# Optimization experiments

Hardware: AMD Instinct MI355X
Metric: run time of the kernel (lower is better)

Reference implementation:

```python
import jax, jax.numpy as jnp
import numpy as np

DIM = 384
RED = 16
PAIR = 128
EPS = 1e-5


def setup_inputs() -> dict:
    key = jax.random.key(0)
    ks = jax.random.split(key, 6)
    b, m = 2, 512
    x = jax.random.normal(ks[0], (b, m, DIM), dtype=jnp.float32)
    ln_gamma = jnp.ones((DIM,), dtype=jnp.float32)
    ln_beta = jnp.zeros((DIM,), dtype=jnp.float32)
    w_red = jax.random.normal(ks[1], (DIM, RED), dtype=jnp.float32) / np.sqrt(DIM)
    b_red = jax.random.normal(ks[2], (RED,), dtype=jnp.float32) * 0.02
    w_out = jax.random.normal(ks[3], (RED * RED, PAIR), dtype=jnp.float32) / np.sqrt(RED * RED)
    b_out = jax.random.normal(ks[4], (PAIR,), dtype=jnp.float32) * 0.02
    return {"x": x, "ln_gamma": ln_gamma, "ln_beta": ln_beta,
            "w_red": w_red, "b_red": b_red, "w_out": w_out, "b_out": b_out}


def reference(x, ln_gamma, ln_beta, w_red, b_red, w_out, b_out):
    # LayerNorm over last dim (eps=1e-5, torch default)
    mu = jnp.mean(x, axis=-1, keepdims=True)
    var = jnp.mean(jnp.square(x - mu), axis=-1, keepdims=True)
    xn = (x - mu) * jax.lax.rsqrt(var + EPS) * ln_gamma + ln_beta
    # Linear dim -> 16
    xr = jnp.einsum('bmd,dr->bmr', xn, w_red) + b_red  # (b, m, 16)
    # Full pairwise outer product + projection: same math as
    # einsum('bmi,bnj->bmnij') -> reshape (i j) -> Linear(256, pair_dim),
    # fused so the (i,j) axes contract directly with w_out reshaped to (16,16,pair).
    wr = w_out.reshape(RED, RED, PAIR)
    out = jnp.einsum('bmi,bnj,ijp->bmnp', xr, xr, wr) + b_out  # (b, m, m, pair)
    return out
```

## Files before the change

### kernel.cpp

```cpp
#include <hip/hip_runtime.h>
#include <hip/hip_bf16.h>

#define DIM 384
#define RED 16
#define PAIR 128
#define B 2
#define M 512
#define EPSV 1e-5f

typedef float f32x4 __attribute__((ext_vector_type(4)));
typedef short bf16x8 __attribute__((ext_vector_type(8)));

__device__ __forceinline__ unsigned short f2bf(float f) {
  union { float f; unsigned u; } v; v.f = f;
  unsigned r = v.u + 0x7fffu + ((v.u >> 16) & 1u);
  return (unsigned short)(r >> 16);
}

__global__ __launch_bounds__(128) void opm_k1(
    const float* __restrict__ x, const float* __restrict__ g,
    const float* __restrict__ be, const float* __restrict__ w_red,
    const float* __restrict__ b_red, const float* __restrict__ w_out,
    unsigned short* __restrict__ xr_bf, unsigned short* __restrict__ T_bf) {
  const int row = blockIdx.x;
  const int tid = threadIdx.x;
  const float* xrow = x + (size_t)row * DIM;

  __shared__ float xn[DIM];
  __shared__ float xr_s[RED];
  __shared__ float rs[2][2];
  __shared__ float psum[8][RED];

  float v0 = xrow[tid];
  float v1 = xrow[tid + 128];
  float v2 = xrow[tid + 256];
  float s  = v0 + v1 + v2;
  float sq = v0 * v0 + v1 * v1 + v2 * v2;
  #pragma unroll
  for (int off = 32; off > 0; off >>= 1) {
    s  += __shfl_down(s, off);
    sq += __shfl_down(sq, off);
  }
  if ((tid & 63) == 0) { rs[0][tid >> 6] = s; rs[1][tid >> 6] = sq; }
  __syncthreads();
  const float mean = (rs[0][0] + rs[0][1]) * (1.0f / DIM);
  const float var  = (rs[1][0] + rs[1][1]) * (1.0f / DIM) - mean * mean;
  const float rstd = rsqrtf(var + EPSV);

  xn[tid]       = (v0 - mean) * rstd * g[tid]       + be[tid];
  xn[tid + 128] = (v1 - mean) * rstd * g[tid + 128] + be[tid + 128];
  xn[tid + 256] = (v2 - mean) * rstd * g[tid + 256] + be[tid + 256];
  __syncthreads();

  {
    const int r = tid & 15;
    const int part = tid >> 4;
    float ps = 0.0f;
    const int d0 = part * 48;
    #pragma unroll 8
    for (int d = d0; d < d0 + 48; ++d) ps += xn[d] * w_red[d * RED + r];
    psum[part][r] = ps;
  }
  __syncthreads();
  if (tid < RED) {
    float v = b_red[tid];
    #pragma unroll
    for (int q = 0; q < 8; ++q) v += psum[q][tid];
    xr_s[tid] = v;
    xr_bf[(size_t)row * RED + tid] = f2bf(v);
  }
  __syncthreads();

  {
    const int p = tid;
    const float* W = w_out + p;
    float acc[RED];
    #pragma unroll
    for (int i = 0; i < RED; ++i) {
      float a = 0.0f;
      #pragma unroll
      for (int j = 0; j < RED; ++j) a += xr_s[j] * W[(i * RED + j) * PAIR];
      acc[i] = a;
    }
    unsigned int w0[4], w1[4];
    #pragma unroll
    for (int k = 0; k < 4; ++k) {
      w0[k] = (unsigned)f2bf(acc[2*k])     | ((unsigned)f2bf(acc[2*k+1]) << 16);
      w1[k] = (unsigned)f2bf(acc[8+2*k])   | ((unsigned)f2bf(acc[8+2*k+1]) << 16);
    }
    unsigned int* dst = (unsigned int*)(T_bf + ((size_t)row * PAIR + p) * RED);
    #pragma unroll
    for (int k = 0; k < 4; ++k) { dst[k] = w0[k]; dst[4+k] = w1[k]; }
  }
}

__global__ __launch_bounds__(256) void opm_k2(
    const unsigned short* __restrict__ xr_bf, const unsigned short* __restrict__ T_bf,
    const float* __restrict__ b_out, float* __restrict__ out) {
  const int nb = blockIdx.x & 127;
  const int mh = (blockIdx.x >> 7) & 1;
  const int b  = blockIdx.x >> 8;
  const int wave = threadIdx.x >> 6;
  const int lane = threadIdx.x & 63;
  const int q = lane >> 4;
  const int r = lane & 15;
  const int n = nb * 4 + wave;

  bf16x8 tv[8];
  const unsigned short* Tb = T_bf + ((size_t)(b * M + n) * PAIR) * RED;
  #pragma unroll
  for (int pb = 0; pb < 8; ++pb) {
    bf16x8 v = {0, 0, 0, 0, 0, 0, 0, 0};
    if (q < 2) v = *(const bf16x8*)(Tb + (pb * 16 + r) * RED + q * 8);
    tv[pb] = v;
  }
  f32x4 biasv[8];
  #pragma unroll
  for (int pb = 0; pb < 8; ++pb)
    biasv[pb] = *(const f32x4*)(b_out + pb * 16 + q * 4);

  const unsigned short* xr_base = xr_bf + (size_t)(b * M) * RED;
  float* out_base = out + ((size_t)(b * M) * M + n) * PAIR + q * 4;

  #pragma unroll
  for (int mt4 = 0; mt4 < 4; ++mt4) {
    const int mt = mh * 4 + mt4;
    #pragma unroll
    for (int ms = 0; ms < 4; ++ms) {
      const int m0 = mt * 64 + ms * 16;
      bf16x8 xv = {0, 0, 0, 0, 0, 0, 0, 0};
      if (q < 2) xv = *(const bf16x8*)(xr_base + (size_t)(m0 + r) * RED + q * 8);

      float* ob = out_base + (size_t)(m0 + r) * M * PAIR;
      #pragma unroll
      for (int pb = 0; pb < 8; ++pb) {
        f32x4 acc = biasv[pb];
        acc = __builtin_amdgcn_mfma_f32_16x16x32_bf16(tv[pb], xv, acc, 0, 0, 0);
        *(f32x4*)(ob + pb * 16) = acc;
      }
    }
  }
}

extern "C" void kernel_launch(void* const* d_in, const int* in_sizes, int n_in,
                              void* d_out, int out_size, void* d_ws, size_t ws_size,
                              hipStream_t stream) {
  const float* x       = (const float*)d_in[0];
  const float* ln_g    = (const float*)d_in[1];
  const float* ln_b    = (const float*)d_in[2];
  const float* w_red   = (const float*)d_in[3];
  const float* b_red   = (const float*)d_in[4];
  const float* w_out   = (const float*)d_in[5];
  const float* b_out   = (const float*)d_in[6];
  float* out = (float*)d_out;

  unsigned short* xr_bf = (unsigned short*)d_ws;
  unsigned short* T_bf  = xr_bf + (size_t)B * M * RED;

  opm_k1<<<B * M, 128, 0, stream>>>(x, ln_g, ln_b, w_red, b_red, w_out, xr_bf, T_bf);
  opm_k2<<<B * (M / 4) * 2, 256, 0, stream>>>(xr_bf, T_bf, b_out, out);
}
```

Measured before the change: 57.45 us.

## Fuse T projection into output kernel via LDS and use wave-per-row LayerNorm

The per-row T = xr·W_out projection moves from the first kernel into the second, where each block builds T for its four n rows in LDS instead of writing it to and reading it back from global workspace. Each T is now computed twice, once per m-half block, in exchange for dropping the T global round trip. The first kernel now handles one row per wave with shuffle-only reductions and no block barriers, and it also writes an fp32 copy of xr for the second kernel.

```diff
diff --git a/kernel.cpp b/kernel.cpp
--- a/kernel.cpp
+++ b/kernel.cpp
@@ -17,101 +17,104 @@
   return (unsigned short)(r >> 16);
 }
 
-__global__ __launch_bounds__(128) void opm_k1(
+__global__ __launch_bounds__(256) void opm_k1(
     const float* __restrict__ x, const float* __restrict__ g,
     const float* __restrict__ be, const float* __restrict__ w_red,
-    const float* __restrict__ b_red, const float* __restrict__ w_out,
-    unsigned short* __restrict__ xr_bf, unsigned short* __restrict__ T_bf) {
-  const int row = blockIdx.x;
-  const int tid = threadIdx.x;
+    const float* __restrict__ b_red,
+    unsigned short* __restrict__ xr_bf, float* __restrict__ xr_f32) {
+  const int wave = threadIdx.x >> 6;
+  const int lane = threadIdx.x & 63;
+  const int row  = blockIdx.x * 4 + wave;
+
+  __shared__ float xn_s[4][DIM];
+
   const float* xrow = x + (size_t)row * DIM;
-
-  __shared__ float xn[DIM];
-  __shared__ float xr_s[RED];
-  __shared__ float rs[2][2];
-  __shared__ float psum[8][RED];
-
-  float v0 = xrow[tid];
-  float v1 = xrow[tid + 128];
-  float v2 = xrow[tid + 256];
-  float s  = v0 + v1 + v2;
-  float sq = v0 * v0 + v1 * v1 + v2 * v2;
+  float v[6];
+  #pragma unroll
+  for (int k = 0; k < 6; ++k) v[k] = xrow[lane + 64 * k];
+  float s = 0.f, sq = 0.f;
+  #pragma unroll
+  for (int k = 0; k < 6; ++k) { s += v[k]; sq += v[k] * v[k]; }
   #pragma unroll
   for (int off = 32; off > 0; off >>= 1) {
-    s  += __shfl_down(s, off);
-    sq += __shfl_down(sq, off);
+    s  += __shfl_xor(s, off);
+    sq += __shfl_xor(sq, off);
   }
-  if ((tid & 63) == 0) { rs[0][tid >> 6] = s; rs[1][tid >> 6] = sq; }
-  __syncthreads();
-  const float mean = (rs[0][0] + rs[0][1]) * (1.0f / DIM);
-  const float var  = (rs[1][0] + rs[1][1]) * (1.0f / DIM) - mean * mean;
+  const float mean = s * (1.0f / DIM);
+  const float var  = sq * (1.0f / DIM) - mean * mean;
   const float rstd = rsqrtf(var + EPSV);
+  #pragma unroll
+  for (int k = 0; k < 6; ++k) {
+    const int d = lane + 64 * k;
+    xn_s[wave][d] = (v[k] - mean) * rstd * g[d] + be[d];
+  }
 
-  xn[tid]       = (v0 - mean) * rstd * g[tid]       + be[tid];
-  xn[tid + 128] = (v1 - mean) * rstd * g[tid + 128] + be[tid + 128];
-  xn[tid + 256] = (v2 - mean) * rstd * g[tid + 256] + be[tid + 256];
-  __syncthreads();
+  const int r = lane & 15, part = lane >> 4;
+  const int d0 = part * 96;
+  float ps = 0.f;
+  #pragma unroll 4
+  for (int d = d0; d < d0 + 96; ++d) ps += xn_s[wave][d] * w_red[d * RED + r];
+  ps += __shfl_xor(ps, 16);
+  ps += __shfl_xor(ps, 32);
+  if (lane < 16) {
+    const float val = ps + b_red[lane];
+    xr_f32[(size_t)row * RED + lane] = val;
+    xr_bf [(size_t)row * RED + lane] = f2bf(val);
+  }
+}
 
-  {
-    const int r = tid & 15;
-    const int part = tid >> 4;
-    float ps = 0.0f;
-    const int d0 = part * 48;
-    #pragma unroll 8
-    for (int d = d0; d < d0 + 48; ++d) ps += xn[d] * w_red[d * RED + r];
-    psum[part][r] = ps;
-  }
-  __syncthreads();
-  if (tid < RED) {
-    float v = b_red[tid];
-    #pragma unroll
-    for (int q = 0; q < 8; ++q) v += psum[q][tid];
-    xr_s[tid] = v;
-    xr_bf[(size_t)row * RED + tid] = f2bf(v);
+__global__ __launch_bounds__(256) void opm_k2(
+    const unsigned short* __restrict__ xr_bf, const float* __restrict__ xr_f32,
+    const float* __restrict__ w_out, const float* __restrict__ b_out,
+    float* __restrict__ out) {
+  const int nb = blockIdx.x & 127;
+  const int mh = (blockIdx.x >> 7) & 1;
+  const int b  = blockIdx.x >> 8;
+  const int tid  = threadIdx.x;
+  const int wave = tid >> 6;
+  const int lane = tid & 63;
+  const int q = lane >> 4;
+  const int r = lane & 15;
+  const int n = nb * 4 + wave;
+
+  __shared__ float xr_lds[4][RED];
+  __shared__ unsigned short T_lds[4][PAIR][RED];
+
+  if (tid < 64) {
+    const int nl = tid >> 4, j = tid & 15;
+    xr_lds[nl][j] = xr_f32[(size_t)(b * M + nb * 4 + nl) * RED + j];
   }
   __syncthreads();
 
   {
-    const int p = tid;
+    const int h2 = tid >> 7;
+    const int p  = tid & 127;
     const float* W = w_out + p;
-    float acc[RED];
+    const float* x0 = xr_lds[2 * h2];
+    const float* x1 = xr_lds[2 * h2 + 1];
+    unsigned int* dst0 = (unsigned int*)&T_lds[2 * h2][p][0];
+    unsigned int* dst1 = (unsigned int*)&T_lds[2 * h2 + 1][p][0];
     #pragma unroll
-    for (int i = 0; i < RED; ++i) {
-      float a = 0.0f;
+    for (int i = 0; i < RED; i += 2) {
+      float a00 = 0.f, a01 = 0.f, a10 = 0.f, a11 = 0.f;
       #pragma unroll
-      for (int j = 0; j < RED; ++j) a += xr_s[j] * W[(i * RED + j) * PAIR];
-      acc[i] = a;
+      for (int j = 0; j < RED; ++j) {
+        const float w0 = W[(i * RED + j) * PAIR];
+        const float w1 = W[((i + 1) * RED + j) * PAIR];
+        a00 += x0[j] * w0;  a01 += x0[j] * w1;
+        a10 += x1[j] * w0;  a11 += x1[j] * w1;
+      }
+      dst0[i >> 1] = (unsigned)f2bf(a00) | ((unsigned)f2bf(a01) << 16);
+      dst1[i >> 1] = (unsigned)f2bf(a10) | ((unsigned)f2bf(a11) << 16);
     }
-    unsigned int w0[4], w1[4];
-    #pragma unroll
-    for (int k = 0; k < 4; ++k) {
-      w0[k] = (unsigned)f2bf(acc[2*k])     | ((unsigned)f2bf(acc[2*k+1]) << 16);
-      w1[k] = (unsigned)f2bf(acc[8+2*k])   | ((unsigned)f2bf(acc[8+2*k+1]) << 16);
-    }
-    unsigned int* dst = (unsigned int*)(T_bf + ((size_t)row * PAIR + p) * RED);
-    #pragma unroll
-    for (int k = 0; k < 4; ++k) { dst[k] = w0[k]; dst[4+k] = w1[k]; }
   }
-}
-
-__global__ __launch_bounds__(256) void opm_k2(
-    const unsigned short* __restrict__ xr_bf, const unsigned short* __restrict__ T_bf,
-    const float* __restrict__ b_out, float* __restrict__ out) {
-  const int nb = blockIdx.x & 127;
-  const int mh = (blockIdx.x >> 7) & 1;
-  const int b  = blockIdx.x >> 8;
-  const int wave = threadIdx.x >> 6;
-  const int lane = threadIdx.x & 63;
-  const int q = lane >> 4;
-  const int r = lane & 15;
-  const int n = nb * 4 + wave;
+  __syncthreads();
 
   bf16x8 tv[8];
-  const unsigned short* Tb = T_bf + ((size_t)(b * M + n) * PAIR) * RED;
   #pragma unroll
   for (int pb = 0; pb < 8; ++pb) {
     bf16x8 v = {0, 0, 0, 0, 0, 0, 0, 0};
-    if (q < 2) v = *(const bf16x8*)(Tb + (pb * 16 + r) * RED + q * 8);
+    if (q < 2) v = *(const bf16x8*)&T_lds[wave][pb * 16 + r][q * 8];
     tv[pb] = v;
   }
   f32x4 biasv[8];
@@ -154,9 +157,9 @@
   const float* b_out   = (const float*)d_in[6];
   float* out = (float*)d_out;
 
-  unsigned short* xr_bf = (unsigned short*)d_ws;
-  unsigned short* T_bf  = xr_bf + (size_t)B * M * RED;
+  unsigned short* xr_bf  = (unsigned short*)d_ws;
+  float*          xr_f32 = (float*)(xr_bf + (size_t)B * M * RED);
 
-  opm_k1<<<B * M, 128, 0, stream>>>(x, ln_g, ln_b, w_red, b_red, w_out, xr_bf, T_bf);
-  opm_k2<<<B * (M / 4) * 2, 256, 0, stream>>>(xr_bf, T_bf, b_out, out);
+  opm_k1<<<B * M / 4, 256, 0, stream>>>(x, ln_g, ln_b, w_red, b_red, xr_bf, xr_f32);
+  opm_k2<<<B * (M / 4) * 2, 256, 0, stream>>>(xr_bf, xr_f32, w_out, b_out, out);
 }
```

New measurement: 63.98 us. 11.4% more time.
